# Performance work log

Hardware: AMD Instinct MI355X
Metric: run time of the kernel (lower is better)

## Reference

```python
import jax, jax.numpy as jnp
import numpy as np

HEADS = 12
HEAD_SIZE = 64
HIDDEN = 768


def _rope_tables(seqlen, dim, dtype):
    inv_freq = 1.0 / (10000.0 ** (jnp.arange(0, dim, 2, dtype=jnp.float32) / dim))
    t = jnp.arange(seqlen, dtype=jnp.float32)
    freqs = t[:, None] * inv_freq[None, :]  # [L, dim/2]
    return jnp.sin(freqs).astype(dtype), jnp.cos(freqs).astype(dtype)


def _apply_rope(x, sin, cos):
    # x: [B, L, H, D]; sin/cos: [L, D/2] -> broadcast as [1, L, 1, D/2]
    sin = sin[None, :, None, :]
    cos = cos[None, :, None, :]
    x1 = x[..., 0::2]
    x2 = x[..., 1::2]
    out1 = x1 * cos - x2 * sin
    out2 = x1 * sin + x2 * cos
    # interleave back: stack on new last axis then flatten
    return jnp.stack([out1, out2], axis=-1).reshape(x.shape)


def setup_inputs() -> dict:
    key = jax.random.key(0)
    k1, k2, k3 = jax.random.split(key, 3)
    B, L = 8, 512
    inputs = jax.random.normal(k1, (B, L, HIDDEN), dtype=jnp.float32)
    attention_mask = jnp.ones((B, L), dtype=jnp.int32)
    out_dim = HEADS * 2 * HEAD_SIZE
    W = jax.random.normal(k2, (HIDDEN, out_dim), dtype=jnp.float32) * (1.0 / np.sqrt(HIDDEN))
    b = jax.random.normal(k3, (out_dim,), dtype=jnp.float32) * 0.02
    return {"inputs": inputs, "W": W, "b": b, "attention_mask": attention_mask}


def reference(inputs, W, b, attention_mask):
    B, L, _ = inputs.shape
    x = inputs @ W + b  # [B, L, H*2*D]
    x = x.reshape(B, L, HEADS, 2, HEAD_SIZE)
    qw = x[..., 0, :]  # [B, L, H, D]
    kw = x[..., 1, :]
    sin, cos = _rope_tables(L, HEAD_SIZE, x.dtype)
    qw = _apply_rope(qw, sin, cos)
    kw = _apply_rope(kw, sin, cos)
    logits = jnp.einsum('bmhd,bnhd->bhmn', qw, kw) / np.sqrt(HEAD_SIZE)
    neg_inf = jnp.finfo(logits.dtype).min
    am = attention_mask.astype(bool)
    valid = am[:, None, None, :] & am[:, None, :, None]
    logits = jnp.where(valid, logits, neg_inf)
    tri = jnp.tril(jnp.ones((L, L), dtype=bool), k=-1)
    logits = jnp.where(tri[None, None, :, :], neg_inf, logits)
    return logits
```

## Files before the change

kernel.cpp:

```cpp
#include <hip/hip_runtime.h>
#include <hip/hip_bf16.h>
#include <math.h>

constexpr int BATCH  = 8;
constexpr int SEQ    = 512;
constexpr int HEADS  = 12;
constexpr int HSIZE  = 64;
constexpr int HIDDEN = 768;
constexpr int OUTD   = 1536;
constexpr int M      = BATCH * SEQ;
constexpr int BH     = BATCH * HEADS;

#define NEG_INF (-3.3895313892515355e38f)

typedef short  s16x8 __attribute__((ext_vector_type(8)));
typedef float  f32x4 __attribute__((ext_vector_type(4)));

__device__ __forceinline__ short f2bf(float f) {
    __hip_bfloat16 h = __float2bfloat16(f);
    return *reinterpret_cast<short*>(&h);
}

__global__ __launch_bounds__(256) void prep_kernel(
    const float* __restrict__ X,  short* __restrict__ Xb,
    const float* __restrict__ W,  short* __restrict__ Wt,
    float* __restrict__ sc_sin,   float* __restrict__ sc_cos)
{
    __shared__ short Ls[32][36];
    const int b   = blockIdx.x;
    const int tid = threadIdx.x;

    if (b < 1536) {
        const int t = b * 256 + tid;
        const float4 a = ((const float4*)X)[t * 2];
        const float4 c = ((const float4*)X)[t * 2 + 1];
        s16x8 o;
        o[0] = f2bf(a.x); o[1] = f2bf(a.y); o[2] = f2bf(a.z); o[3] = f2bf(a.w);
        o[4] = f2bf(c.x); o[5] = f2bf(c.y); o[6] = f2bf(c.z); o[7] = f2bf(c.w);
        ((s16x8*)Xb)[t] = o;
    } else if (b < 2688) {
        const int bid = b - 1536;
        const int nx = bid % 48, ky = bid / 48;
        const int r  = tid >> 3;
        const int c4 = (tid & 7) * 4;
        const float4 v = *(const float4*)(W + (size_t)(ky * 32 + r) * OUTD + nx * 32 + c4);
        Ls[r][c4 + 0] = f2bf(v.x); Ls[r][c4 + 1] = f2bf(v.y);
        Ls[r][c4 + 2] = f2bf(v.z); Ls[r][c4 + 3] = f2bf(v.w);
        __syncthreads();
        short o0 = Ls[c4 + 0][r], o1 = Ls[c4 + 1][r];
        short o2 = Ls[c4 + 2][r], o3 = Ls[c4 + 3][r];
        short* dst = Wt + (size_t)(nx * 32 + r) * HIDDEN + ky * 32 + c4;
        dst[0] = o0; dst[1] = o1; dst[2] = o2; dst[3] = o3;
    } else {
        const int t   = (b - 2688) * 256 + tid;
        const int pos = t >> 5, pi = t & 31;
        const float invf = exp2f((float)(2 * pi) * (-13.287712379549449f / 64.0f));
        const float ang  = (float)pos * invf;
        sc_sin[t] = sinf(ang);
        sc_cos[t] = cosf(ang);
    }
}

__global__ __launch_bounds__(256) void proj_mfma_kernel(
    const short* __restrict__ Xb,
    const short* __restrict__ Wt,
    const float* __restrict__ bias,
    const float* __restrict__ sc_sin,
    const float* __restrict__ sc_cos,
    short* __restrict__ Qb,
    short* __restrict__ Kb)
{
    union Sh {
        struct { short As[2][128 * 64]; short Bs[2][64 * 64]; } st;
        float epi[128 * 68];
    };
    __shared__ Sh sh;

    const int tid = threadIdx.x;
    const int l   = tid & 63;
    const int w   = tid >> 6;
    const int mBase = blockIdx.y * 128;
    const int nBase = blockIdx.x * 64;
    const int wm = w * 32;

    const int r0  = tid >> 3;
    const int g   = tid & 7;
    const int gsw = (g ^ (r0 & 7)) * 8;

    s16x8 ar[4], br[2];
#pragma unroll
    for (int p = 0; p < 4; ++p)
        ar[p] = *(const s16x8*)(Xb + (size_t)(mBase + r0 + p * 32) * HIDDEN + g * 8);
#pragma unroll
    for (int p = 0; p < 2; ++p)
        br[p] = *(const s16x8*)(Wt + (size_t)(nBase + r0 + p * 32) * HIDDEN + g * 8);

#pragma unroll
    for (int p = 0; p < 4; ++p)
        *(s16x8*)(sh.st.As[0] + (r0 + p * 32) * 64 + gsw) = ar[p];
#pragma unroll
    for (int p = 0; p < 2; ++p)
        *(s16x8*)(sh.st.Bs[0] + (r0 + p * 32) * 64 + gsw) = br[p];

    f32x4 acc[2][4] = {};
    int buf = 0;

    for (int k0 = 0; k0 < HIDDEN; k0 += 64) {
        __syncthreads();
        const bool more = (k0 + 64 < HIDDEN);
        if (more) {
#pragma unroll
            for (int p = 0; p < 4; ++p)
                ar[p] = *(const s16x8*)(Xb + (size_t)(mBase + r0 + p * 32) * HIDDEN + (k0 + 64) + g * 8);
#pragma unroll
            for (int p = 0; p < 2; ++p)
                br[p] = *(const s16x8*)(Wt + (size_t)(nBase + r0 + p * 32) * HIDDEN + (k0 + 64) + g * 8);
        }
        const short* Asb = sh.st.As[buf];
        const short* Bsb = sh.st.Bs[buf];
#pragma unroll
        for (int s = 0; s < 2; ++s) {
            const int c = ((s * 4 + (l >> 4)) ^ (l & 7)) * 8;
            s16x8 af[2], bf[4];
#pragma unroll
            for (int i = 0; i < 2; ++i)
                af[i] = *(const s16x8*)(Asb + (wm + i * 16 + (l & 15)) * 64 + c);
#pragma unroll
            for (int j = 0; j < 4; ++j)
                bf[j] = *(const s16x8*)(Bsb + (j * 16 + (l & 15)) * 64 + c);
#pragma unroll
            for (int i = 0; i < 2; ++i)
#pragma unroll
                for (int j = 0; j < 4; ++j)
                    acc[i][j] = __builtin_amdgcn_mfma_f32_16x16x32_bf16(
                        af[i], bf[j], acc[i][j], 0, 0, 0);
        }
        if (more) {
            const int nb = buf ^ 1;
#pragma unroll
            for (int p = 0; p < 4; ++p)
                *(s16x8*)(sh.st.As[nb] + (r0 + p * 32) * 64 + gsw) = ar[p];
#pragma unroll
            for (int p = 0; p < 2; ++p)
                *(s16x8*)(sh.st.Bs[nb] + (r0 + p * 32) * 64 + gsw) = br[p];
            buf = nb;
        }
    }

    __syncthreads();

    const int colL = l & 15, quad = l >> 4;
#pragma unroll
    for (int j = 0; j < 4; ++j) {
        const int nl = j * 16 + colL;
#pragma unroll
        for (int i = 0; i < 2; ++i)
#pragma unroll
            for (int r = 0; r < 4; ++r)
                sh.epi[(wm + i * 16 + quad * 4 + r) * 68 + nl] = acc[i][j][r];
    }
    __syncthreads();

    const int bb   = mBase >> 9;
    const int pos0 = mBase & 511;
    const int h    = nBase >> 7;
    const int slot = (nBase >> 6) & 1;
    short* dst = (slot ? Kb : Qb) + ((size_t)(bb * HEADS + h) * SEQ + pos0) * HSIZE;

#pragma unroll
    for (int p = 0; p < 4; ++p) {
        const int c    = tid + p * 256;
        const int mrow = c >> 3;
        const int ch   = c & 7;
        const int dloc = ch * 8;
        const int pos  = pos0 + mrow;

        const float* src = &sh.epi[mrow * 68 + dloc];
        const float4 v0 = *(const float4*)(src);
        const float4 v1 = *(const float4*)(src + 4);
        const float* bp = bias + nBase + dloc;
        const float4 b0 = *(const float4*)(bp);
        const float4 b1 = *(const float4*)(bp + 4);
        const float4 sn = *(const float4*)(sc_sin + pos * 32 + (dloc >> 1));
        const float4 cs = *(const float4*)(sc_cos + pos * 32 + (dloc >> 1));

        const float e0 = v0.x + b0.x, o0 = v0.y + b0.y;
        const float e1 = v0.z + b0.z, o1 = v0.w + b0.w;
        const float e2 = v1.x + b1.x, o2 = v1.y + b1.y;
        const float e3 = v1.z + b1.z, o3 = v1.w + b1.w;
        s16x8 ov;
        ov[0] = f2bf(e0 * cs.x - o0 * sn.x); ov[1] = f2bf(e0 * sn.x + o0 * cs.x);
        ov[2] = f2bf(e1 * cs.y - o1 * sn.y); ov[3] = f2bf(e1 * sn.y + o1 * cs.y);
        ov[4] = f2bf(e2 * cs.z - o2 * sn.z); ov[5] = f2bf(e2 * sn.z + o2 * cs.z);
        ov[6] = f2bf(e3 * cs.w - o3 * sn.w); ov[7] = f2bf(e3 * sn.w + o3 * cs.w);
        *(s16x8*)(dst + (size_t)mrow * HSIZE + dloc) = ov;
    }
}

__global__ __launch_bounds__(256) void qk_mfma_kernel(
    const short* __restrict__ Qb,
    const short* __restrict__ Kb,
    const int*   __restrict__ am,
    float* __restrict__ out)
{
    const int bh = blockIdx.z;
    const int bb = bh / HEADS;
    const int m0 = blockIdx.y * 128;
    const int n0 = blockIdx.x * 128;
    const int tid = threadIdx.x;

    if (m0 >= n0 + 128) {
        const float4 ninf = make_float4(NEG_INF, NEG_INF, NEG_INF, NEG_INF);
        float* base = out + ((size_t)bh * SEQ + m0) * SEQ + n0;
        const int c = (tid & 31) * 4;
#pragma unroll
        for (int r = 0; r < 16; ++r) {
            const int row = r * 8 + (tid >> 5);
            *(float4*)(base + (size_t)row * SEQ + c) = ninf;
        }
        return;
    }

    __shared__ short Qs[128 * 64];
    __shared__ short Ks[128 * 64];
    __shared__ __align__(16) int amR[128];
    __shared__ __align__(16) int amC[128];

    const int l = tid & 63;
    const int w = tid >> 6;
    if (tid < 128)      amR[tid]       = am[bb * SEQ + m0 + tid];
    else                amC[tid - 128] = am[bb * SEQ + n0 + (tid - 128)];

    const int r0  = tid >> 3;
    const int g   = tid & 7;
    const int gsw = (g ^ (r0 & 7)) * 8;
#pragma unroll
    for (int p = 0; p < 4; ++p) {
        const int row = r0 + p * 32;
        const s16x8 qv = *(const s16x8*)(Qb + ((size_t)bh * SEQ + m0 + row) * HSIZE + g * 8);
        const s16x8 kv = *(const s16x8*)(Kb + ((size_t)bh * SEQ + n0 + row) * HSIZE + g * 8);
        *(s16x8*)(Qs + row * 64 + gsw) = qv;
        *(s16x8*)(Ks + row * 64 + gsw) = kv;
    }
    __syncthreads();

    const int wm = (w & 1) * 64;
    const int wn = (w >> 1) * 64;
    f32x4 acc[4][4] = {};
#pragma unroll
    for (int s = 0; s < 2; ++s) {
        const int c = ((s * 4 + (l >> 4)) ^ (l & 7)) * 8;
        s16x8 qf[4], kf[4];
#pragma unroll
        for (int i = 0; i < 4; ++i) {
            qf[i] = *(const s16x8*)(Qs + (wm + i * 16 + (l & 15)) * 64 + c);
            kf[i] = *(const s16x8*)(Ks + (wn + i * 16 + (l & 15)) * 64 + c);
        }
#pragma unroll
        for (int i = 0; i < 4; ++i)
#pragma unroll
            for (int j = 0; j < 4; ++j)
                acc[i][j] = __builtin_amdgcn_mfma_f32_16x16x32_bf16(
                    qf[i], kf[j], acc[i][j], 0, 0, 0);
    }

    const int colL = l & 15, quad = l >> 4;
    int rm[4][4];
#pragma unroll
    for (int i = 0; i < 4; ++i)
#pragma unroll
        for (int r = 0; r < 4; ++r)
            rm[i][r] = amR[wm + i * 16 + quad * 4 + r];

#pragma unroll
    for (int j = 0; j < 4; ++j) {
        const int nl = wn + j * 16 + colL;
        const int ng = n0 + nl;
        const int an = amC[nl];
#pragma unroll
        for (int i = 0; i < 4; ++i) {
#pragma unroll
            for (int r = 0; r < 4; ++r) {
                const int ml = wm + i * 16 + quad * 4 + r;
                const int mg = m0 + ml;
                float v = acc[i][j][r] * 0.125f;
                if (ng < mg || !an || !rm[i][r]) v = NEG_INF;
                out[((size_t)bh * SEQ + mg) * SEQ + ng] = v;
            }
        }
    }
}

extern "C" void kernel_launch(void* const* d_in, const int* in_sizes, int n_in,
                              void* d_out, int out_size, void* d_ws, size_t ws_size,
                              hipStream_t stream) {
    const float* X    = (const float*)d_in[0];
    const float* W    = (const float*)d_in[1];
    const float* bias = (const float*)d_in[2];
    const int*   am   = (const int*)d_in[3];
    float* out = (float*)d_out;

    char* ws = (char*)d_ws;
    short* Xb = (short*)(ws);
    short* Wt = (short*)(ws + 6291456);
    short* Qb = (short*)(ws + 8650752);
    short* Kb = (short*)(ws + 14942208);
    float* sc_sin = (float*)(ws + 21233664);
    float* sc_cos = (float*)(ws + 21299200);

    prep_kernel<<<dim3(2752), 256, 0, stream>>>(X, Xb, W, Wt, sc_sin, sc_cos);
    proj_mfma_kernel<<<dim3(OUTD / 64, M / 128), 256, 0, stream>>>(
        Xb, Wt, bias, sc_sin, sc_cos, Qb, Kb);
    qk_mfma_kernel<<<dim3(SEQ / 128, SEQ / 128, BH), 256, 0, stream>>>(Qb, Kb, am, out);
}
```

Measured before the change: 153.6 us.

## Use direct global-to-LDS loads for GEMM and logits tile staging

Replaces register-staged global loads plus LDS stores with the global_load_lds builtin (16-byte direct-to-LDS) in both the projection GEMM and the logits kernel. The read address is XOR-permuted so the existing swizzled LDS layout is preserved, and the GEMM double-buffer loop is restructured to issue the next stage before computing with one barrier per iteration. The aim is to cut VGPR pressure and LDS write instructions and to overlap loads with MFMA. The W transpose store is also vectorised to short4. Correctness relies on the barrier waiting for the async LDS writes, and 16-byte direct-LDS loads need gfx950 support.

```diff
diff --git a/kernel.cpp b/kernel.cpp
--- a/kernel.cpp
+++ b/kernel.cpp
@@ -1,6 +1,7 @@
 #include <hip/hip_runtime.h>
 #include <hip/hip_bf16.h>
 #include <math.h>
+#include <stdint.h>
 
 constexpr int BATCH  = 8;
 constexpr int SEQ    = 512;
@@ -19,6 +20,15 @@
 __device__ __forceinline__ short f2bf(float f) {
     __hip_bfloat16 h = __float2bfloat16(f);
     return *reinterpret_cast<short*>(&h);
+}
+
+__device__ __forceinline__ void g2l16(const void* g, void* l) {
+    __builtin_amdgcn_global_load_lds(
+        reinterpret_cast<const __attribute__((address_space(1))) int*>(
+            reinterpret_cast<uintptr_t>(g)),
+        reinterpret_cast<__attribute__((address_space(3))) int*>(
+            reinterpret_cast<uintptr_t>(l)),
+        16, 0, 0);
 }
 
 __global__ __launch_bounds__(256) void prep_kernel(
@@ -47,10 +57,10 @@
         Ls[r][c4 + 0] = f2bf(v.x); Ls[r][c4 + 1] = f2bf(v.y);
         Ls[r][c4 + 2] = f2bf(v.z); Ls[r][c4 + 3] = f2bf(v.w);
         __syncthreads();
-        short o0 = Ls[c4 + 0][r], o1 = Ls[c4 + 1][r];
-        short o2 = Ls[c4 + 2][r], o3 = Ls[c4 + 3][r];
-        short* dst = Wt + (size_t)(nx * 32 + r) * HIDDEN + ky * 32 + c4;
-        dst[0] = o0; dst[1] = o1; dst[2] = o2; dst[3] = o3;
+        short4 ov;
+        ov.x = Ls[c4 + 0][r]; ov.y = Ls[c4 + 1][r];
+        ov.z = Ls[c4 + 2][r]; ov.w = Ls[c4 + 3][r];
+        *(short4*)(Wt + (size_t)(nx * 32 + r) * HIDDEN + ky * 32 + c4) = ov;
     } else {
         const int t   = (b - 2688) * 256 + tid;
         const int pos = t >> 5, pi = t & 31;
@@ -83,39 +93,32 @@
     const int nBase = blockIdx.x * 64;
     const int wm = w * 32;
 
-    const int r0  = tid >> 3;
-    const int g   = tid & 7;
-    const int gsw = (g ^ (r0 & 7)) * 8;
-
-    s16x8 ar[4], br[2];
-#pragma unroll
-    for (int p = 0; p < 4; ++p)
-        ar[p] = *(const s16x8*)(Xb + (size_t)(mBase + r0 + p * 32) * HIDDEN + g * 8);
-#pragma unroll
-    for (int p = 0; p < 2; ++p)
-        br[p] = *(const s16x8*)(Wt + (size_t)(nBase + r0 + p * 32) * HIDDEN + g * 8);
-
-#pragma unroll
-    for (int p = 0; p < 4; ++p)
-        *(s16x8*)(sh.st.As[0] + (r0 + p * 32) * 64 + gsw) = ar[p];
-#pragma unroll
-    for (int p = 0; p < 2; ++p)
-        *(s16x8*)(sh.st.Bs[0] + (r0 + p * 32) * 64 + gsw) = br[p];
+    const int lr = l >> 3;
+    const int gc = (l & 7) ^ lr;
+    const short* aSrc = Xb + (size_t)(mBase + wm + lr)     * HIDDEN + gc * 8;
+    const short* bSrc = Wt + (size_t)(nBase + w * 16 + lr) * HIDDEN + gc * 8;
+
+#define STAGE(buf_, k0_)                                                     \
+    do {                                                                     \
+        _Pragma("unroll")                                                    \
+        for (int p = 0; p < 4; ++p)                                          \
+            g2l16(aSrc + (k0_) + p * 8 * HIDDEN,                             \
+                  sh.st.As[buf_] + (w * 4 + p) * 512);                       \
+        _Pragma("unroll")                                                    \
+        for (int p = 0; p < 2; ++p)                                          \
+            g2l16(bSrc + (k0_) + p * 8 * HIDDEN,                             \
+                  sh.st.Bs[buf_] + (w * 2 + p) * 512);                       \
+    } while (0)
+
+    STAGE(0, 0);
+    __syncthreads();
 
     f32x4 acc[2][4] = {};
     int buf = 0;
 
     for (int k0 = 0; k0 < HIDDEN; k0 += 64) {
-        __syncthreads();
-        const bool more = (k0 + 64 < HIDDEN);
-        if (more) {
-#pragma unroll
-            for (int p = 0; p < 4; ++p)
-                ar[p] = *(const s16x8*)(Xb + (size_t)(mBase + r0 + p * 32) * HIDDEN + (k0 + 64) + g * 8);
-#pragma unroll
-            for (int p = 0; p < 2; ++p)
-                br[p] = *(const s16x8*)(Wt + (size_t)(nBase + r0 + p * 32) * HIDDEN + (k0 + 64) + g * 8);
-        }
+        if (k0 + 64 < HIDDEN)
+            STAGE(buf ^ 1, k0 + 64);
         const short* Asb = sh.st.As[buf];
         const short* Bsb = sh.st.Bs[buf];
 #pragma unroll
@@ -135,19 +138,10 @@
                     acc[i][j] = __builtin_amdgcn_mfma_f32_16x16x32_bf16(
                         af[i], bf[j], acc[i][j], 0, 0, 0);
         }
-        if (more) {
-            const int nb = buf ^ 1;
-#pragma unroll
-            for (int p = 0; p < 4; ++p)
-                *(s16x8*)(sh.st.As[nb] + (r0 + p * 32) * 64 + gsw) = ar[p];
-#pragma unroll
-            for (int p = 0; p < 2; ++p)
-                *(s16x8*)(sh.st.Bs[nb] + (r0 + p * 32) * 64 + gsw) = br[p];
-            buf = nb;
-        }
-    }
-
-    __syncthreads();
+        __syncthreads();
+        buf ^= 1;
+    }
+#undef STAGE
 
     const int colL = l & 15, quad = l >> 4;
 #pragma unroll
@@ -231,16 +225,14 @@
     if (tid < 128)      amR[tid]       = am[bb * SEQ + m0 + tid];
     else                amC[tid - 128] = am[bb * SEQ + n0 + (tid - 128)];
 
-    const int r0  = tid >> 3;
-    const int g   = tid & 7;
-    const int gsw = (g ^ (r0 & 7)) * 8;
+    const int lr = l >> 3;
+    const int gc = (l & 7) ^ lr;
+    const short* qSrc = Qb + ((size_t)bh * SEQ + m0 + w * 32 + lr) * HSIZE + gc * 8;
+    const short* kSrc = Kb + ((size_t)bh * SEQ + n0 + w * 32 + lr) * HSIZE + gc * 8;
 #pragma unroll
     for (int p = 0; p < 4; ++p) {
-        const int row = r0 + p * 32;
-        const s16x8 qv = *(const s16x8*)(Qb + ((size_t)bh * SEQ + m0 + row) * HSIZE + g * 8);
-        const s16x8 kv = *(const s16x8*)(Kb + ((size_t)bh * SEQ + n0 + row) * HSIZE + g * 8);
-        *(s16x8*)(Qs + row * 64 + gsw) = qv;
-        *(s16x8*)(Ks + row * 64 + gsw) = kv;
+        g2l16(qSrc + p * 8 * HSIZE, Qs + (w * 4 + p) * 512);
+        g2l16(kSrc + p * 8 * HSIZE, Ks + (w * 4 + p) * 512);
     }
     __syncthreads();
 
```

Measured after the change: 144.3 us. -6.1%, faster.
